# Performance work log

Measured on AMD Instinct MI355X. Metric: run time of the kernel, lower is better.

## Reference

```python
import jax, jax.numpy as jnp
import numpy as np

B, S, D, H, DH = 2, 2048, 1024, 16, 64

def setup_inputs() -> dict:
    key = jax.random.key(0)
    ks = jax.random.split(key, 9)
    sc = 0.02
    return {
        "x":  jax.random.normal(ks[0], (B, S, D), jnp.float32),
        "Wq": jax.random.normal(ks[1], (H, D, DH), jnp.float32) * sc,
        "bq": jax.random.normal(ks[2], (H, DH), jnp.float32) * sc,
        "Wk": jax.random.normal(ks[3], (H, D, DH), jnp.float32) * sc,
        "bk": jax.random.normal(ks[4], (H, DH), jnp.float32) * sc,
        "Wv": jax.random.normal(ks[5], (H, D, DH), jnp.float32) * sc,
        "bv": jax.random.normal(ks[6], (H, DH), jnp.float32) * sc,
        "Wo": jax.random.normal(ks[7], (D, D), jnp.float32) * sc,
        "bo": jax.random.normal(ks[8], (D,), jnp.float32) * sc,
    }

def reference(x, Wq, bq, Wk, bk, Wv, bv, Wo, bo):
    # Fused version of the per-head Python loop: all H heads batched.
    # q,k,v: [B,H,S,DH]
    q = jnp.einsum("bsi,hid->bhsd", x, Wq) + bq[None, :, None, :]
    k = jnp.einsum("bsi,hid->bhsd", x, Wk) + bk[None, :, None, :]
    v = jnp.einsum("bsi,hid->bhsd", x, Wv) + bv[None, :, None, :]
    scale = 1.0 / jnp.sqrt(jnp.asarray(DH, x.dtype))
    scores = jnp.einsum("bhsd,bhtd->bhst", q, k) * scale  # [B,H,S,S]
    attn = jax.nn.softmax(scores, axis=-1)
    o = jnp.einsum("bhst,bhtd->bhsd", attn, v)            # [B,H,S,DH]
    # torch.cat([head_0,...,head_{H-1}], dim=-1) -> [B,S,H*DH]
    o = jnp.transpose(o, (0, 2, 1, 3)).reshape(B, S, H * DH)
    # Dropout is identity in eval mode; final dense projection.
    return jnp.einsum("bsi,io->bso", o, Wo) + bo
```

## Files before the change

### kernel.cpp

```cpp
#include <hip/hip_runtime.h>
#include <hip/hip_bf16.h>

#define BB 2
#define SS 2048
#define DD 1024
#define HH 16
#define DHH 64

typedef __attribute__((ext_vector_type(8))) __bf16 bf16x8;
typedef __attribute__((ext_vector_type(4))) float f32x4;
typedef __attribute__((ext_vector_type(16))) float f32x16;
typedef __attribute__((ext_vector_type(4))) int i32x4;
typedef __attribute__((ext_vector_type(4))) unsigned int u32x4;

#define MFMA16 __builtin_amdgcn_mfma_f32_16x16x32_bf16
#define MFMA32 __builtin_amdgcn_mfma_f32_32x32x16_bf16

__device__ __forceinline__ unsigned short f2b(float f) {
  __hip_bfloat16 h = __float2bfloat16(f);
  unsigned short u;
  __builtin_memcpy(&u, &h, 2);
  return u;
}

__device__ __forceinline__ float b2f(unsigned short u) {
  unsigned int x = ((unsigned int)u) << 16;
  float f;
  __builtin_memcpy(&f, &x, 4);
  return f;
}

__device__ __forceinline__ float exp2_fast(float x) {
  float r;
  asm("v_exp_f32 %0, %1" : "=v"(r) : "v"(x));
  return r;
}

__device__ __forceinline__ unsigned int cvtpk_bf16(float lo_, float hi_) {
  unsigned int r;
  asm("v_cvt_pk_bf16_f32 %0, %1, %2" : "=v"(r) : "v"(lo_), "v"(hi_));
  return r;
}

__device__ __forceinline__ void gl_lds16(const void* g, void* l) {
  __builtin_amdgcn_global_load_lds((const __attribute__((address_space(1))) void*)g,
                                   (__attribute__((address_space(3))) void*)l, 16, 0, 0);
}

__global__ __launch_bounds__(256) void k_prep(const float* __restrict__ x,
                                              const float* __restrict__ Wq,
                                              const float* __restrict__ Wk,
                                              const float* __restrict__ Wv,
                                              const float* __restrict__ Wo,
                                              unsigned short* __restrict__ xb,
                                              unsigned short* __restrict__ wqkvt,
                                              unsigned short* __restrict__ wot) {
  int blk = blockIdx.x;
  if (blk < 4096) {
    int i = blk * 256 + threadIdx.x;
    float4 v = ((const float4*)x)[i];
    ushort4 o;
    o.x = f2b(v.x); o.y = f2b(v.y); o.z = f2b(v.z); o.w = f2b(v.w);
    ((ushort4*)xb)[i] = o;
    return;
  }
  __shared__ float t[32][33];
  const float* im;
  unsigned short* om;
  int R, C, c0, r0;
  if (blk < 7168) {
    int bi2 = blk - 4096;
    int z = bi2 >> 6, rem = bi2 & 63;
    im = (z < 16 ? Wq : (z < 32 ? Wk : Wv)) + (size_t)(z & 15) * DD * DHH;
    om = wqkvt + (size_t)z * DD * DHH;
    R = DD; C = DHH;
    c0 = (rem & 1) * 32; r0 = (rem >> 1) * 32;
  } else {
    int bi2 = blk - 7168;
    im = Wo; om = wot;
    R = DD; C = DD;
    c0 = (bi2 & 31) * 32; r0 = (bi2 >> 5) * 32;
  }
  int tx = threadIdx.x & 31, ty = threadIdx.x >> 5;
#pragma unroll
  for (int rr = ty; rr < 32; rr += 8)
    t[rr][tx] = im[(size_t)(r0 + rr) * C + c0 + tx];
  __syncthreads();
#pragma unroll
  for (int rr = ty; rr < 32; rr += 8)
    om[(size_t)(c0 + rr) * R + r0 + tx] = f2b(t[tx][rr]);
}

__global__ __launch_bounds__(256, 2) void k_qkv(const unsigned short* __restrict__ A,
                                                const unsigned short* __restrict__ Wt,
                                                const float* __restrict__ bq,
                                                const float* __restrict__ bk,
                                                const float* __restrict__ bv,
                                                unsigned short* __restrict__ Qb,
                                                unsigned short* __restrict__ Kb,
                                                unsigned short* __restrict__ Vtb) {
  __shared__ __align__(16) unsigned short SMEM[3 * 12288];
  int tid = threadIdx.x;
  int w = tid >> 6, l = tid & 63, lr = l & 15, lg = l >> 4;
  int col0 = blockIdx.x * 64, row0 = blockIdx.y * 128;
  int sel = col0 >> 10;
  bool vsel = (sel == 2);
  const float* biasp = sel == 0 ? bq : (sel == 1 ? bk : bv);
  unsigned short* outp = sel == 0 ? Qb : Kb;
  float qscale = sel == 0 ? 0.18033688011112042f : 1.0f;

  int r8 = l >> 3, c8 = l & 7;
  const unsigned short* Ab = A + (size_t)(row0 + w * 32 + r8) * DD + (c8 ^ r8) * 8;
  const unsigned short* Bb = Wt + (size_t)(col0 + w * 16 + r8) * DD + (c8 ^ r8) * 8;
  const int swr = (lr & 7) << 4;

  f32x4 zero = {0.f, 0.f, 0.f, 0.f};
  f32x4 acc[2][4];
#pragma unroll
  for (int m = 0; m < 2; m++)
#pragma unroll
    for (int n = 0; n < 4; n++) acc[m][n] = zero;

#define QKV_STAGE(T) do { \
    unsigned short* buf_ = SMEM + ((T) % 3) * 12288; \
    int k0_ = (T) * 64; \
    _Pragma("unroll") \
    for (int c = 0; c < 4; c++) \
      gl_lds16(Ab + (size_t)c * 8 * DD + k0_, (char*)buf_ + (w * 32 + c * 8) * 128); \
    _Pragma("unroll") \
    for (int c = 0; c < 2; c++) \
      gl_lds16(Bb + (size_t)c * 8 * DD + k0_, (char*)(buf_ + 8192) + (w * 16 + c * 8) * 128); \
  } while (0)

#define QKV_COMPUTE(T) do { \
    const char* As_ = (const char*)(SMEM + ((T) % 3) * 12288); \
    const char* Bs_ = As_ + 16384; \
    _Pragma("unroll") \
    for (int kk = 0; kk < 2; kk++) { \
      int co_ = (kk * 64 + lg * 16) ^ swr; \
      bf16x8 af[2], bfr[4]; \
      _Pragma("unroll") \
      for (int m = 0; m < 2; m++) \
        af[m] = *(const bf16x8*)(As_ + (w * 32 + m * 16 + lr) * 128 + co_); \
      _Pragma("unroll") \
      for (int n = 0; n < 4; n++) \
        bfr[n] = *(const bf16x8*)(Bs_ + (n * 16 + lr) * 128 + co_); \
      if (!vsel) { \
        _Pragma("unroll") \
        for (int m = 0; m < 2; m++) \
          _Pragma("unroll") \
          for (int n = 0; n < 4; n++) \
            acc[m][n] = MFMA16(af[m], bfr[n], acc[m][n], 0, 0, 0); \
      } else { \
        _Pragma("unroll") \
        for (int m = 0; m < 2; m++) \
          _Pragma("unroll") \
          for (int n = 0; n < 4; n++) \
            acc[m][n] = MFMA16(bfr[n], af[m], acc[m][n], 0, 0, 0); \
      } \
    } \
  } while (0)

  QKV_STAGE(0);
  QKV_STAGE(1);
  for (int t = 0; t < 15; t++) {
    asm volatile("s_waitcnt vmcnt(6) lgkmcnt(0)" ::: "memory");
    __builtin_amdgcn_s_barrier();
    if (t + 2 < 16) QKV_STAGE(t + 2);
    QKV_COMPUTE(t);
  }
  asm volatile("s_waitcnt vmcnt(0) lgkmcnt(0)" ::: "memory");
  __builtin_amdgcn_s_barrier();
  QKV_COMPUTE(15);
#undef QKV_STAGE
#undef QKV_COMPUTE

  __syncthreads();
  unsigned short* Ts = SMEM;
  if (!vsel) {
#pragma unroll
    for (int n = 0; n < 4; n++) {
      int cl = n * 16 + lr;
      float bias = biasp[(col0 + cl) & 1023];
#pragma unroll
      for (int m = 0; m < 2; m++) {
#pragma unroll
        for (int j = 0; j < 4; j++) {
          int sl = w * 32 + m * 16 + lg * 4 + j;
          Ts[sl * 72 + cl] = f2b((acc[m][n][j] + bias) * qscale);
        }
      }
    }
    __syncthreads();
    int trow = tid >> 3, tc = tid & 7;
#pragma unroll
    for (int pass = 0; pass < 4; pass++) {
      int sl = pass * 32 + trow;
      int c0l = tc * 8;
      i32x4 v = *(const i32x4*)&Ts[sl * 72 + c0l];
      int c = col0 + c0l;
      int hh = (c >> 6) & 15, d = c & 63;
      int row = row0 + sl;
      int b = row >> 11, s = row & 2047;
      *(i32x4*)(outp + ((size_t)(b * HH + hh) * SS + s) * DHH + d) = v;
    }
  } else {
#pragma unroll
    for (int n = 0; n < 4; n++) {
#pragma unroll
      for (int j = 0; j < 4; j++) {
        int cl = n * 16 + lg * 4 + j;
        float bias = bv[((col0 & 1023) + cl) & 1023];
#pragma unroll
        for (int m = 0; m < 2; m++) {
          int sl = w * 32 + m * 16 + lr;
          Ts[cl * 136 + sl] = f2b(acc[m][n][j] + bias);
        }
      }
    }
    __syncthreads();
    int trow = tid >> 4, tc = tid & 15;
    int b = row0 >> 11, s0 = row0 & 2047;
#pragma unroll
    for (int pass = 0; pass < 4; pass++) {
      int cl = pass * 16 + trow;
      int s8 = tc * 8;
      i32x4 v = *(const i32x4*)&Ts[cl * 136 + s8];
      int cg = (col0 & 1023) + cl;
      *(i32x4*)(Vtb + (size_t)(b * 1024 + cg) * SS + s0 + s8) = v;
    }
  }
}

__global__ __launch_bounds__(256, 3) void k_proj(const unsigned short* __restrict__ A,
                                                 const unsigned short* __restrict__ Wt,
                                                 const float* __restrict__ bo,
                                                 float* __restrict__ out) {
  __shared__ __align__(16) unsigned short SMEM[3 * 8192];
  int tid = threadIdx.x;
  int w = tid >> 6, l = tid & 63, lr = l & 15, lg = l >> 4;
  int col0 = blockIdx.x * 64, row0 = blockIdx.y * 64;

  int r8 = l >> 3, c8 = l & 7;
  const unsigned short* Ab = A + (size_t)(row0 + w * 16 + r8) * DD + (c8 ^ r8) * 8;
  const unsigned short* Bb = Wt + (size_t)(col0 + w * 16 + r8) * DD + (c8 ^ r8) * 8;
  const int swr = (lr & 7) << 4;

  f32x4 zero = {0.f, 0.f, 0.f, 0.f};
  f32x4 acc[4];
#pragma unroll
  for (int n = 0; n < 4; n++) acc[n] = zero;

#define PROJ_STAGE(T) do { \
    unsigned short* buf_ = SMEM + ((T) % 3) * 8192; \
    int k0_ = (T) * 64; \
    _Pragma("unroll") \
    for (int c = 0; c < 2; c++) { \
      gl_lds16(Ab + (size_t)c * 8 * DD + k0_, (char*)buf_ + (w * 16 + c * 8) * 128); \
      gl_lds16(Bb + (size_t)c * 8 * DD + k0_, (char*)(buf_ + 4096) + (w * 16 + c * 8) * 128); \
    } \
  } while (0)

#define PROJ_COMPUTE(T) do { \
    const char* As_ = (const char*)(SMEM + ((T) % 3) * 8192); \
    const char* Bs_ = As_ + 8192; \
    _Pragma("unroll") \
    for (int kk = 0; kk < 2; kk++) { \
      int co_ = (kk * 64 + lg * 16) ^ swr; \
      bf16x8 af = *(const bf16x8*)(As_ + (w * 16 + lr) * 128 + co_); \
      bf16x8 bfr[4]; \
      _Pragma("unroll") \
      for (int n = 0; n < 4; n++) \
        bfr[n] = *(const bf16x8*)(Bs_ + (n * 16 + lr) * 128 + co_); \
      _Pragma("unroll") \
      for (int n = 0; n < 4; n++) \
        acc[n] = MFMA16(af, bfr[n], acc[n], 0, 0, 0); \
    } \
  } while (0)

  PROJ_STAGE(0);
  PROJ_STAGE(1);
  for (int t = 0; t < 15; t++) {
    asm volatile("s_waitcnt vmcnt(4) lgkmcnt(0)" ::: "memory");
    __builtin_amdgcn_s_barrier();
    if (t + 2 < 16) PROJ_STAGE(t + 2);
    PROJ_COMPUTE(t);
  }
  asm volatile("s_waitcnt vmcnt(0) lgkmcnt(0)" ::: "memory");
  __builtin_amdgcn_s_barrier();
  PROJ_COMPUTE(15);
#undef PROJ_STAGE
#undef PROJ_COMPUTE

#pragma unroll
  for (int n = 0; n < 4; n++) {
    int c = col0 + n * 16 + lr;
    float bias = bo[c];
#pragma unroll
    for (int j = 0; j < 4; j++) {
      int row = row0 + w * 16 + lg * 4 + j;
      out[(size_t)row * DD + c] = acc[n][j] + bias;
    }
  }
}

#define QT 128
#define KVB 64

__global__ __launch_bounds__(256, 4) void k_attn(const unsigned short* __restrict__ Q,
                                                 const unsigned short* __restrict__ K,
                                                 const unsigned short* __restrict__ Vt,
                                                 unsigned short* __restrict__ Opart,
                                                 float* __restrict__ lse) {
  __shared__ __align__(16) char sm[32768];

  int tid = threadIdx.x;
  int w = tid >> 6, lane = tid & 63;
  int q32 = lane & 31, hi = lane >> 5;
  int r8 = lane >> 3, c8 = lane & 7;
  int cg = c8 ^ r8;

  int n = blockIdx.x;
  int bh = ((n & 7) << 2) | ((n >> 3) & 3);
  int rest = n >> 5;
  int q0 = (rest & 15) * QT;
  int chunk = rest >> 4;
  int kvbase = chunk * (SS / 2);

  const unsigned short* Qm = Q + (size_t)bh * SS * DHH;
  const unsigned short* Km = K + (size_t)bh * SS * DHH;
  const unsigned short* Vm = Vt + (size_t)bh * DHH * SS;

  bf16x8 qf[4];
  {
    const unsigned short* qrow = Qm + (size_t)(q0 + w * 32 + q32) * DHH + hi * 8;
#pragma unroll
    for (int ks = 0; ks < 4; ks++)
      qf[ks] = *(const bf16x8*)(qrow + ks * 16);
  }

#pragma unroll
  for (int c = 0; c < 2; c++) {
    int rr = w * 16 + c * 8 + r8;
    gl_lds16(Km + (size_t)(kvbase + rr) * DHH + cg * 8, sm + (w * 16 + c * 8) * 128);
    gl_lds16(Vm + (size_t)rr * SS + kvbase + cg * 8, sm + 16384 + (w * 16 + c * 8) * 128);
  }
  __syncthreads();

  const f32x16 FZERO = {};
  f32x16 oacc0 = FZERO, oacc1 = FZERO;
  float m_ = -1e30f, l_ = 0.f;
  const int swq = (q32 & 7) << 4;

  for (int t = 0; t < SS / 2 / KVB; t++) {
    const char* Kc = sm + (t & 1) * 8192;
    const char* Vc = sm + 16384 + (t & 1) * 8192;

    if (t + 1 < SS / 2 / KVB) {
      int kv0 = kvbase + (t + 1) * KVB;
      char* kd = sm + ((t + 1) & 1) * 8192;
      char* vd = sm + 16384 + ((t + 1) & 1) * 8192;
#pragma unroll
      for (int c = 0; c < 2; c++) {
        int rr = w * 16 + c * 8 + r8;
        gl_lds16(Km + (size_t)(kv0 + rr) * DHH + cg * 8, kd + (w * 16 + c * 8) * 128);
        gl_lds16(Vm + (size_t)rr * SS + kv0 + cg * 8, vd + (w * 16 + c * 8) * 128);
      }
    }

    f32x16 p0, p1;
    __builtin_amdgcn_s_setprio(1);
    {
      int co = (hi * 16) ^ swq;
      bf16x8 kf0 = *(const bf16x8*)(Kc + q32 * 128 + co);
      bf16x8 kf1 = *(const bf16x8*)(Kc + (32 + q32) * 128 + co);
      p0 = MFMA32(kf0, qf[0], FZERO, 0, 0, 0);
      p1 = MFMA32(kf1, qf[0], FZERO, 0, 0, 0);
    }
#pragma unroll
    for (int ks = 1; ks < 4; ks++) {
      int co = (ks * 32 + hi * 16) ^ swq;
      bf16x8 kf0 = *(const bf16x8*)(Kc + q32 * 128 + co);
      bf16x8 kf1 = *(const bf16x8*)(Kc + (32 + q32) * 128 + co);
      p0 = MFMA32(kf0, qf[ks], p0, 0, 0, 0);
      p1 = MFMA32(kf1, qf[ks], p1, 0, 0, 0);
    }
    __builtin_amdgcn_s_setprio(0);

    float t8[8];
#pragma unroll
    for (int r = 0; r < 8; r++)
      t8[r] = fmaxf(fmaxf(p0[r], p0[r + 8]), fmaxf(p1[r], p1[r + 8]));
#pragma unroll
    for (int r = 0; r < 4; r++) t8[r] = fmaxf(t8[r], t8[r + 4]);
    float tmax = fmaxf(fmaxf(t8[0], t8[1]), fmaxf(t8[2], t8[3]));
    tmax = fmaxf(tmax, __shfl_xor(tmax, 32));

    if (__any(tmax > m_ + 8.0f)) {
      float nm = fmaxf(m_, tmax);
      float al = exp2_fast(m_ - nm);
      m_ = nm; l_ *= al;
#pragma unroll
      for (int r = 0; r < 16; r++) { oacc0[r] *= al; oacc1[r] *= al; }
    }

#pragma unroll
    for (int r = 0; r < 16; r++) p0[r] = exp2_fast(p0[r] - m_);
#pragma unroll
    for (int r = 0; r < 16; r++) p1[r] = exp2_fast(p1[r] - m_);
    float s8[8];
#pragma unroll
    for (int r = 0; r < 8; r++) s8[r] = (p0[r] + p0[r + 8]) + (p1[r] + p1[r + 8]);
#pragma unroll
    for (int r = 0; r < 4; r++) s8[r] += s8[r + 4];
    l_ += ((s8[0] + s8[1]) + (s8[2] + s8[3]));

    __builtin_amdgcn_s_setprio(1);
    u32x4 pa;
#define MKPA(PB, u) do { \
    unsigned int a0 = cvtpk_bf16(PB[8*(u)+0], PB[8*(u)+1]); \
    unsigned int a1 = cvtpk_bf16(PB[8*(u)+2], PB[8*(u)+3]); \
    unsigned int b0 = cvtpk_bf16(PB[8*(u)+4], PB[8*(u)+5]); \
    unsigned int b1 = cvtpk_bf16(PB[8*(u)+6], PB[8*(u)+7]); \
    asm("v_permlane32_swap_b32 %0, %1" : "+v"(a0), "+v"(b0)); \
    asm("v_permlane32_swap_b32 %0, %1" : "+v"(a1), "+v"(b1)); \
    pa[0] = a0; pa[1] = a1; pa[2] = b0; pa[3] = b1; \
  } while (0)
#define PVSTEP(s) do { \
    bf16x8 pf = *(bf16x8*)&pa; \
    bf16x8 vf0 = *(const bf16x8*)(Vc + q32 * 128 + (((s) * 32 + hi * 16) ^ swq)); \
    bf16x8 vf1 = *(const bf16x8*)(Vc + (32 + q32) * 128 + (((s) * 32 + hi * 16) ^ swq)); \
    oacc0 = MFMA32(vf0, pf, oacc0, 0, 0, 0); \
    oacc1 = MFMA32(vf1, pf, oacc1, 0, 0, 0); \
  } while (0)
    MKPA(p0, 0); PVSTEP(0);
    MKPA(p0, 1); PVSTEP(1);
    MKPA(p1, 0); PVSTEP(2);
    MKPA(p1, 1); PVSTEP(3);
#undef MKPA
#undef PVSTEP
    __builtin_amdgcn_s_setprio(0);

    __syncthreads();
  }

  l_ += __shfl_xor(l_, 32);
  float invl = 1.0f / l_;
  float lsev = m_ + __log2f(l_);
  __syncthreads();
  unsigned short* Os = (unsigned short*)sm;
  int rowq = w * 32 + q32;
#pragma unroll
  for (int r = 0; r < 16; r++) {
    int d = (r & 3) + 8 * (r >> 2) + 4 * hi;
    Os[rowq * 72 + d] = f2b(oacc0[r] * invl);
    Os[rowq * 72 + 32 + d] = f2b(oacc1[r] * invl);
  }
  if (hi == 0) lse[((size_t)chunk * 32 + bh) * SS + q0 + rowq] = lsev;
  __syncthreads();
#pragma unroll
  for (int i = 0; i < 4; i++) {
    int ci = tid + i * 256;
    int r = ci >> 3, c = ci & 7;
    i32x4 v = *(const i32x4*)&Os[r * 72 + c * 8];
    *(i32x4*)(Opart + (((size_t)chunk * 32 + bh) * SS + q0 + r) * DHH + c * 8) = v;
  }
}

__global__ __launch_bounds__(256) void k_comb(const unsigned short* __restrict__ Opart,
                                              const float* __restrict__ lse,
                                              unsigned short* __restrict__ Ocat) {
  int g = blockIdx.x * 256 + threadIdx.x;
  int row = g >> 3;
  int d8 = (g & 7) * 8;
  int bh = row >> 11, q = row & 2047;
  int bi = bh >> 4, h = bh & 15;
  float e0 = lse[row], e1 = lse[BB * HH * SS + row];
  float mx = fmaxf(e0, e1);
  float w0 = exp2_fast(e0 - mx), w1 = exp2_fast(e1 - mx);
  float inv = 1.0f / (w0 + w1);
  w0 *= inv; w1 *= inv;
  const unsigned short* P0 = Opart + (size_t)row * DHH + d8;
  const unsigned short* P1 = P0 + (size_t)BB * HH * SS * DHH;
  ushort4 a0 = *(const ushort4*)P0, a1 = *(const ushort4*)(P0 + 4);
  ushort4 b0 = *(const ushort4*)P1, b1 = *(const ushort4*)(P1 + 4);
  ushort4 o0, o1;
  o0.x = f2b(w0 * b2f(a0.x) + w1 * b2f(b0.x));
  o0.y = f2b(w0 * b2f(a0.y) + w1 * b2f(b0.y));
  o0.z = f2b(w0 * b2f(a0.z) + w1 * b2f(b0.z));
  o0.w = f2b(w0 * b2f(a0.w) + w1 * b2f(b0.w));
  o1.x = f2b(w0 * b2f(a1.x) + w1 * b2f(b1.x));
  o1.y = f2b(w0 * b2f(a1.y) + w1 * b2f(b1.y));
  o1.z = f2b(w0 * b2f(a1.z) + w1 * b2f(b1.z));
  o1.w = f2b(w0 * b2f(a1.w) + w1 * b2f(b1.w));
  unsigned short* op = Ocat + ((size_t)(bi * SS + q)) * DD + h * DHH + d8;
  *(ushort4*)op = o0;
  *(ushort4*)(op + 4) = o1;
}

extern "C" void kernel_launch(void* const* d_in, const int* in_sizes, int n_in,
                              void* d_out, int out_size, void* d_ws, size_t ws_size,
                              hipStream_t stream) {
  const float* x  = (const float*)d_in[0];
  const float* Wq = (const float*)d_in[1];
  const float* bq = (const float*)d_in[2];
  const float* Wk = (const float*)d_in[3];
  const float* bk = (const float*)d_in[4];
  const float* Wv = (const float*)d_in[5];
  const float* bv = (const float*)d_in[6];
  const float* Wo = (const float*)d_in[7];
  const float* bo = (const float*)d_in[8];
  float* out = (float*)d_out;

  char* ws = (char*)d_ws;
  unsigned short* xb    = (unsigned short*)(ws);
  unsigned short* wqkvt = (unsigned short*)(ws + (size_t)(8u  << 20));
  unsigned short* wot   = (unsigned short*)(ws + (size_t)(14u << 20));
  unsigned short* Qb    = (unsigned short*)(ws + (size_t)(16u << 20));
  unsigned short* Kb    = (unsigned short*)(ws + (size_t)(24u << 20));
  unsigned short* Vt    = (unsigned short*)(ws + (size_t)(32u << 20));
  unsigned short* Ocat  = (unsigned short*)(ws + (size_t)(40u << 20));
  unsigned short* Opart = (unsigned short*)(ws + (size_t)(48u << 20));
  float*          lse   = (float*)(ws + (size_t)(64u << 20));

  k_prep<<<8192, 256, 0, stream>>>(x, Wq, Wk, Wv, Wo, xb, wqkvt, wot);
  k_qkv<<<dim3(3 * DD / 64, BB * SS / 128), 256, 0, stream>>>(xb, wqkvt, bq, bk, bv, Qb, Kb, Vt);
  k_attn<<<dim3(1024), 256, 0, stream>>>(Qb, Kb, Vt, Opart, lse);
  k_comb<<<dim3(2048), 256, 0, stream>>>(Opart, lse, Ocat);
  k_proj<<<dim3(DD / 64, BB * SS / 64), 256, 0, stream>>>(Ocat, wot, bo, out);
}
```

Baseline: 113.4 us.

## Retile QKV GEMM to 128x128 block tiles with 2x2 warp layout and BK=32

The QKV projection kernel now uses 128x128 output tiles per block, with four waves arranged 2x2, each computing a 64x64 sub-tile. The K step shrinks from 64 to 32, so the shared-memory stages and XOR swizzle change to match, and occupancy is raised to 3 blocks per SM. The goal is more operand reuse per LDS load and less redundant global traffic, since fewer column blocks each re-read x. In exchange the grid halves to 768 blocks, each wave holds more accumulator registers, and there are twice as many pipeline iterations and barriers.

```diff
diff --git a/kernel.cpp b/kernel.cpp
--- a/kernel.cpp
+++ b/kernel.cpp
@@ -91,7 +91,7 @@
     om[(size_t)(c0 + rr) * R + r0 + tx] = f2b(t[tx][rr]);
 }
 
-__global__ __launch_bounds__(256, 2) void k_qkv(const unsigned short* __restrict__ A,
+__global__ __launch_bounds__(256, 3) void k_qkv(const unsigned short* __restrict__ A,
                                                 const unsigned short* __restrict__ Wt,
                                                 const float* __restrict__ bq,
                                                 const float* __restrict__ bk,
@@ -99,79 +99,78 @@
                                                 unsigned short* __restrict__ Qb,
                                                 unsigned short* __restrict__ Kb,
                                                 unsigned short* __restrict__ Vtb) {
-  __shared__ __align__(16) unsigned short SMEM[3 * 12288];
+  __shared__ __align__(16) unsigned short SMEM[3 * 8192];
   int tid = threadIdx.x;
   int w = tid >> 6, l = tid & 63, lr = l & 15, lg = l >> 4;
-  int col0 = blockIdx.x * 64, row0 = blockIdx.y * 128;
+  int wr = w >> 1, wc = w & 1;
+  int col0 = blockIdx.x * 128, row0 = blockIdx.y * 128;
   int sel = col0 >> 10;
   bool vsel = (sel == 2);
   const float* biasp = sel == 0 ? bq : (sel == 1 ? bk : bv);
   unsigned short* outp = sel == 0 ? Qb : Kb;
   float qscale = sel == 0 ? 0.18033688011112042f : 1.0f;
 
-  int r8 = l >> 3, c8 = l & 7;
-  const unsigned short* Ab = A + (size_t)(row0 + w * 32 + r8) * DD + (c8 ^ r8) * 8;
-  const unsigned short* Bb = Wt + (size_t)(col0 + w * 16 + r8) * DD + (c8 ^ r8) * 8;
-  const int swr = (lr & 7) << 4;
+  int r16 = l >> 2, c4 = l & 3;
+  int cg = c4 ^ ((r16 >> 1) & 3);
+  const unsigned short* Ab = A + (size_t)(row0 + w * 32 + r16) * DD + cg * 8;
+  const unsigned short* Bb = Wt + (size_t)(col0 + w * 32 + r16) * DD + cg * 8;
+  const int swr = ((lr >> 1) & 3) << 4;
 
   f32x4 zero = {0.f, 0.f, 0.f, 0.f};
-  f32x4 acc[2][4];
-#pragma unroll
-  for (int m = 0; m < 2; m++)
+  f32x4 acc[4][4];
+#pragma unroll
+  for (int m = 0; m < 4; m++)
 #pragma unroll
     for (int n = 0; n < 4; n++) acc[m][n] = zero;
 
 #define QKV_STAGE(T) do { \
-    unsigned short* buf_ = SMEM + ((T) % 3) * 12288; \
-    int k0_ = (T) * 64; \
-    _Pragma("unroll") \
-    for (int c = 0; c < 4; c++) \
-      gl_lds16(Ab + (size_t)c * 8 * DD + k0_, (char*)buf_ + (w * 32 + c * 8) * 128); \
+    unsigned short* buf_ = SMEM + ((T) % 3) * 8192; \
+    int k0_ = (T) * 32; \
     _Pragma("unroll") \
     for (int c = 0; c < 2; c++) \
-      gl_lds16(Bb + (size_t)c * 8 * DD + k0_, (char*)(buf_ + 8192) + (w * 16 + c * 8) * 128); \
+      gl_lds16(Ab + (size_t)c * 16 * DD + k0_, (char*)buf_ + (w * 32 + c * 16) * 64); \
+    _Pragma("unroll") \
+    for (int c = 0; c < 2; c++) \
+      gl_lds16(Bb + (size_t)c * 16 * DD + k0_, (char*)(buf_ + 4096) + (w * 32 + c * 16) * 64); \
   } while (0)
 
 #define QKV_COMPUTE(T) do { \
-    const char* As_ = (const char*)(SMEM + ((T) % 3) * 12288); \
-    const char* Bs_ = As_ + 16384; \
+    const char* As_ = (const char*)(SMEM + ((T) % 3) * 8192); \
+    const char* Bs_ = As_ + 8192; \
+    int co_ = (lg * 16) ^ swr; \
+    bf16x8 af[4], bfr[4]; \
     _Pragma("unroll") \
-    for (int kk = 0; kk < 2; kk++) { \
-      int co_ = (kk * 64 + lg * 16) ^ swr; \
-      bf16x8 af[2], bfr[4]; \
+    for (int m = 0; m < 4; m++) \
+      af[m] = *(const bf16x8*)(As_ + (wr * 64 + m * 16 + lr) * 64 + co_); \
+    _Pragma("unroll") \
+    for (int n = 0; n < 4; n++) \
+      bfr[n] = *(const bf16x8*)(Bs_ + (wc * 64 + n * 16 + lr) * 64 + co_); \
+    if (!vsel) { \
       _Pragma("unroll") \
-      for (int m = 0; m < 2; m++) \
-        af[m] = *(const bf16x8*)(As_ + (w * 32 + m * 16 + lr) * 128 + co_); \
+      for (int m = 0; m < 4; m++) \
+        _Pragma("unroll") \
+        for (int n = 0; n < 4; n++) \
+          acc[m][n] = MFMA16(af[m], bfr[n], acc[m][n], 0, 0, 0); \
+    } else { \
       _Pragma("unroll") \
-      for (int n = 0; n < 4; n++) \
-        bfr[n] = *(const bf16x8*)(Bs_ + (n * 16 + lr) * 128 + co_); \
-      if (!vsel) { \
+      for (int m = 0; m < 4; m++) \
         _Pragma("unroll") \
-        for (int m = 0; m < 2; m++) \
-          _Pragma("unroll") \
-          for (int n = 0; n < 4; n++) \
-            acc[m][n] = MFMA16(af[m], bfr[n], acc[m][n], 0, 0, 0); \
-      } else { \
-        _Pragma("unroll") \
-        for (int m = 0; m < 2; m++) \
-          _Pragma("unroll") \
-          for (int n = 0; n < 4; n++) \
-            acc[m][n] = MFMA16(bfr[n], af[m], acc[m][n], 0, 0, 0); \
-      } \
+        for (int n = 0; n < 4; n++) \
+          acc[m][n] = MFMA16(bfr[n], af[m], acc[m][n], 0, 0, 0); \
     } \
   } while (0)
 
   QKV_STAGE(0);
   QKV_STAGE(1);
-  for (int t = 0; t < 15; t++) {
-    asm volatile("s_waitcnt vmcnt(6) lgkmcnt(0)" ::: "memory");
+  for (int t = 0; t < 31; t++) {
+    asm volatile("s_waitcnt vmcnt(4) lgkmcnt(0)" ::: "memory");
     __builtin_amdgcn_s_barrier();
-    if (t + 2 < 16) QKV_STAGE(t + 2);
+    if (t + 2 < 32) QKV_STAGE(t + 2);
     QKV_COMPUTE(t);
   }
   asm volatile("s_waitcnt vmcnt(0) lgkmcnt(0)" ::: "memory");
   __builtin_amdgcn_s_barrier();
-  QKV_COMPUTE(15);
+  QKV_COMPUTE(31);
 #undef QKV_STAGE
 #undef QKV_COMPUTE
 
@@ -180,24 +179,24 @@
   if (!vsel) {
 #pragma unroll
     for (int n = 0; n < 4; n++) {
-      int cl = n * 16 + lr;
+      int cl = wc * 64 + n * 16 + lr;
       float bias = biasp[(col0 + cl) & 1023];
 #pragma unroll
-      for (int m = 0; m < 2; m++) {
+      for (int m = 0; m < 4; m++) {
 #pragma unroll
         for (int j = 0; j < 4; j++) {
-          int sl = w * 32 + m * 16 + lg * 4 + j;
-          Ts[sl * 72 + cl] = f2b((acc[m][n][j] + bias) * qscale);
+          int sl = wr * 64 + m * 16 + lg * 4 + j;
+          Ts[sl * 136 + cl] = f2b((acc[m][n][j] + bias) * qscale);
         }
       }
     }
     __syncthreads();
-    int trow = tid >> 3, tc = tid & 7;
-#pragma unroll
-    for (int pass = 0; pass < 4; pass++) {
-      int sl = pass * 32 + trow;
+    int trow = tid >> 4, tc = tid & 15;
+#pragma unroll
+    for (int pass = 0; pass < 8; pass++) {
+      int sl = pass * 16 + trow;
       int c0l = tc * 8;
-      i32x4 v = *(const i32x4*)&Ts[sl * 72 + c0l];
+      i32x4 v = *(const i32x4*)&Ts[sl * 136 + c0l];
       int c = col0 + c0l;
       int hh = (c >> 6) & 15, d = c & 63;
       int row = row0 + sl;
@@ -209,11 +208,11 @@
     for (int n = 0; n < 4; n++) {
 #pragma unroll
       for (int j = 0; j < 4; j++) {
-        int cl = n * 16 + lg * 4 + j;
+        int cl = wc * 64 + n * 16 + lg * 4 + j;
         float bias = bv[((col0 & 1023) + cl) & 1023];
 #pragma unroll
-        for (int m = 0; m < 2; m++) {
-          int sl = w * 32 + m * 16 + lr;
+        for (int m = 0; m < 4; m++) {
+          int sl = wr * 64 + m * 16 + lr;
           Ts[cl * 136 + sl] = f2b(acc[m][n][j] + bias);
         }
       }
@@ -222,12 +221,12 @@
     int trow = tid >> 4, tc = tid & 15;
     int b = row0 >> 11, s0 = row0 & 2047;
 #pragma unroll
-    for (int pass = 0; pass < 4; pass++) {
+    for (int pass = 0; pass < 8; pass++) {
       int cl = pass * 16 + trow;
       int s8 = tc * 8;
       i32x4 v = *(const i32x4*)&Ts[cl * 136 + s8];
-      int cg = (col0 & 1023) + cl;
-      *(i32x4*)(Vtb + (size_t)(b * 1024 + cg) * SS + s0 + s8) = v;
+      int cg2 = (col0 & 1023) + cl;
+      *(i32x4*)(Vtb + (size_t)(b * 1024 + cg2) * SS + s0 + s8) = v;
     }
   }
 }
@@ -524,7 +523,7 @@
   float*          lse   = (float*)(ws + (size_t)(64u << 20));
 
   k_prep<<<8192, 256, 0, stream>>>(x, Wq, Wk, Wv, Wo, xb, wqkvt, wot);
-  k_qkv<<<dim3(3 * DD / 64, BB * SS / 128), 256, 0, stream>>>(xb, wqkvt, bq, bk, bv, Qb, Kb, Vt);
+  k_qkv<<<dim3(3 * DD / 128, BB * SS / 128), 256, 0, stream>>>(xb, wqkvt, bq, bk, bv, Qb, Kb, Vt);
   k_attn<<<dim3(1024), 256, 0, stream>>>(Qb, Kb, Vt, Opart, lse);
   k_comb<<<dim3(2048), 256, 0, stream>>>(Opart, lse, Ocat);
   k_proj<<<dim3(DD / 64, BB * SS / 64), 256, 0, stream>>>(Ocat, wot, bo, out);
```

New measurement: 116.7 us. 1.03x slower.
